# Kernel optimization log

Hardware: AMD Instinct MI355X
Metric: run time of the kernel (lower is better)

Reference implementation:

```python
import jax, jax.numpy as jnp
import numpy as np

RADIUS = 400.0
FIELD = 8000.0  # um extent of slide coordinate field


def setup_inputs() -> dict:
    key = jax.random.key(0)
    ks = jax.random.split(key, 8)
    B, N, D, H, K = 4, 4096, 1536, 512, 8
    images = jax.random.normal(ks[0], (B, N, D), dtype=jnp.float32)
    positions = jax.random.uniform(ks[1], (B, N, 2), dtype=jnp.float32) * FIELD
    W_feat = jax.random.normal(ks[2], (D, H), dtype=jnp.float32) * (1.0 / np.sqrt(D))
    b_feat = jnp.zeros((H,), dtype=jnp.float32)
    W_pos = jax.random.normal(ks[3], (2, H), dtype=jnp.float32) * 0.5
    W_gnn = jax.random.normal(ks[4], (H, H), dtype=jnp.float32) * (1.0 / np.sqrt(H))
    W_self = jax.random.normal(ks[5], (H, H), dtype=jnp.float32) * (1.0 / np.sqrt(H))
    anchors = jax.random.normal(ks[6], (K, D), dtype=jnp.float32)
    return {"images": images, "positions": positions, "W_feat": W_feat,
            "b_feat": b_feat, "W_pos": W_pos, "W_gnn": W_gnn,
            "W_self": W_self, "anchors": anchors}


def _radius_adjacency(pos):
    # pos: (N, 2). Dense O(N^2) radius graph (mirrors torch.cdist + mask).
    sq = jnp.sum(pos * pos, axis=-1)                       # (N,)
    d2 = sq[:, None] + sq[None, :] - 2.0 * (pos @ pos.T)   # (N, N)
    mask = d2 < (RADIUS * RADIUS)
    N = pos.shape[0]
    mask = mask & ~jnp.eye(N, dtype=bool)                  # no self-loops
    return mask.astype(pos.dtype)


def reference(images, positions, W_feat, b_feat, W_pos, W_gnn, W_self, anchors):
    # --- Stream A: explicit concept quantifier (cosine sim to anchors) ---
    x_norm = images / jnp.clip(jnp.linalg.norm(images, axis=-1, keepdims=True), 1e-12)
    a_norm = anchors / jnp.clip(jnp.linalg.norm(anchors, axis=-1, keepdims=True), 1e-12)
    scores = jnp.einsum('bnd,kd->bnk', x_norm, a_norm)     # (B, N, K)
    concept_profile = scores.mean(axis=1)                  # (B, K)

    # --- Stream B: feature extraction with positional encoding ---
    feat = images @ W_feat + b_feat + positions @ W_pos    # (B, N, H)

    # --- radius graph + one mean-aggregation GNN layer, per slide ---
    def per_graph(f, p):
        A = _radius_adjacency(p)                           # (N, N)
        deg = jnp.clip(A.sum(axis=-1, keepdims=True), 1.0) # (N, 1)
        h = jax.nn.relu(f)
        agg = (A @ h) / deg                                # mean over neighbors
        return jax.nn.relu(agg @ W_gnn + f @ W_self)       # (N, H)

    refined = jax.vmap(per_graph)(feat, positions)         # (B, N, H)
    latent_spatial = refined.mean(axis=1)                  # (B, H)  per-graph mean pool

    return jnp.concatenate([latent_spatial, concept_profile], axis=1)  # (B, H+K)
```

## Files before the change

kernel.cpp:

```cpp
#include <hip/hip_runtime.h>

#define B_ 4
#define N_ 4096
#define D_ 1536
#define H_ 512
#define K_ 8
#define M_ (B_*N_)
#define R2_ 160000.0f
#define CAP 192

typedef __attribute__((ext_vector_type(8))) short bf16x8;
typedef __attribute__((ext_vector_type(4))) float f32x4;
typedef __attribute__((ext_vector_type(2))) float f32x2;

__device__ __forceinline__ unsigned short f2bf(float f) {
  union { float f; unsigned u; } v; v.f = f;
  unsigned r = (v.u + 0x7FFFu + ((v.u >> 16) & 1u)) >> 16;
  return (unsigned short)r;
}

typedef const __attribute__((address_space(1))) unsigned int gas_u32;
typedef __attribute__((address_space(3))) unsigned int las_u32;
__device__ __forceinline__ void gl_lds16(const unsigned short* g, unsigned short* l) {
  __builtin_amdgcn_global_load_lds((gas_u32*)g, (las_u32*)l, 16, 0, 0);
}

#define CAST_BLKS 4096

__global__ __launch_bounds__(256) void k_prepcast(
    const float* __restrict__ images, const float* __restrict__ anchors,
    const float* __restrict__ Wf, const float* __restrict__ Wg, const float* __restrict__ Ws,
    unsigned short* __restrict__ imgs_bf, float* __restrict__ inv_norm,
    unsigned short* __restrict__ WfT, unsigned short* __restrict__ WgsT,
    unsigned short* __restrict__ ancT, float* __restrict__ invanorm) {
  int tid = threadIdx.x;
  if (blockIdx.x >= CAST_BLKS) {
    int bi = blockIdx.x - CAST_BLKS;
    if (bi < 320) {
      __shared__ float t[64][65];
      int bx = bi & 7, by = bi >> 3;
      const float* W; unsigned short* WT; int kt, outStride, outOff;
      if (by < 24)      { W = Wf; WT = WfT;  kt = by;      outStride = D_;   outOff = 0; }
      else if (by < 32) { W = Wg; WT = WgsT; kt = by - 24; outStride = 1024; outOff = 0; }
      else              { W = Ws; WT = WgsT; kt = by - 32; outStride = 1024; outOff = 512; }
      int tx = tid & 63, ty = tid >> 6;
      #pragma unroll
      for (int r = 0; r < 64; r += 4)
        t[ty + r][tx] = W[(size_t)(kt*64 + ty + r)*H_ + bx*64 + tx];
      __syncthreads();
      #pragma unroll
      for (int r = 0; r < 64; r += 4) {
        int n = bx*64 + ty + r;
        WT[(size_t)n*outStride + outOff + kt*64 + tx] = f2bf(t[tx][ty + r]);
      }
      return;
    }
    __shared__ float red[4];
    int k = bi - 320;
    float s = 0.f;
    for (int i = tid; i < D_; i += 256) {
      float v = anchors[k*D_ + i];
      s += v*v;
      ancT[(size_t)k*D_ + i] = f2bf(v);
      ancT[(size_t)(k+8)*D_ + i] = 0;
    }
    #pragma unroll
    for (int off = 32; off; off >>= 1) s += __shfl_down(s, off);
    if ((tid & 63) == 0) red[tid >> 6] = s;
    __syncthreads();
    if (tid == 0) invanorm[k] = 1.0f / fmaxf(sqrtf(red[0]+red[1]+red[2]+red[3]), 1e-12f);
    return;
  }
  int lane = tid & 63, w = tid >> 6;
  int row = blockIdx.x*4 + w;
  const float4* xr = (const float4*)(images + (size_t)row*D_);
  ushort4* ob = (ushort4*)(imgs_bf + (size_t)row*D_);
  float nrm = 0.f;
  #pragma unroll
  for (int it = 0; it < 6; it++) {
    float4 x = xr[lane + 64*it];
    nrm += x.x*x.x + x.y*x.y + x.z*x.z + x.w*x.w;
    ushort4 s;
    s.x = f2bf(x.x); s.y = f2bf(x.y); s.z = f2bf(x.z); s.w = f2bf(x.w);
    ob[lane + 64*it] = s;
  }
  #pragma unroll
  for (int off = 32; off; off >>= 1) nrm += __shfl_down(nrm, off);
  if (lane == 0) inv_norm[row] = 1.0f / fmaxf(sqrtf(nrm), 1e-12f);
}

#define BM 128
#define BN 128
#define BK 32

__global__ __launch_bounds__(256) void k_gemm(
    const unsigned short* __restrict__ A, const unsigned short* __restrict__ BT,
    int Kdim, int mode, const float* __restrict__ bias, const float* __restrict__ Wpos,
    const float* __restrict__ positions, unsigned short* __restrict__ AB,
    unsigned char* __restrict__ P, const unsigned short* __restrict__ ancT,
    const float* __restrict__ invnorm, const float* __restrict__ invanorm,
    float* __restrict__ out) {
  __shared__ __align__(16) unsigned short As[2][BM*BK];
  __shared__ __align__(16) unsigned short Bs[2][BN*BK];
  __shared__ float colsum[BN];
  int tid = threadIdx.x;
  int lane = tid & 63, wv = tid >> 6;
  int l15 = lane & 15, quad = lane >> 4;
  int bx = blockIdx.x;

  int wm = wv >> 1, wn = wv & 1;
  int j = bx >> 3;
  int bm = (bx & 7) + 8*(j >> 2), bn = j & 3;
  int m0 = bm*BM, n0 = bn*BN;

  const bool doC = (mode == 0) && (bn == 0);

  f32x4 acc[4][4] = {};
  f32x4 cacc[2] = {};
  const unsigned short* anc = ancT + l15*D_ + quad*8;

  int c = wv*2;
  int rowc = (lane >> 2), seg = lane & 3;
  const unsigned short* gA0 = A  + (size_t)(m0 + c*16 + rowc)*Kdim + seg*8;
  const unsigned short* gA1 = gA0 + (size_t)16*Kdim;
  const unsigned short* gB0 = BT + (size_t)(n0 + c*16 + rowc)*Kdim + seg*8;
  const unsigned short* gB1 = gB0 + (size_t)16*Kdim;

  int nk = Kdim / BK;
  gl_lds16(gA0, As[0] + c*512); gl_lds16(gA1, As[0] + c*512 + 512);
  gl_lds16(gB0, Bs[0] + c*512); gl_lds16(gB1, Bs[0] + c*512 + 512);
  gA0 += BK; gA1 += BK; gB0 += BK; gB1 += BK;
  __syncthreads();

  int cur = 0;
  for (int kt = 0; kt < nk; kt++) {
    if (kt + 1 < nk) {
      unsigned short* nA = As[cur ^ 1] + c*512;
      unsigned short* nB = Bs[cur ^ 1] + c*512;
      gl_lds16(gA0, nA); gl_lds16(gA1, nA + 512);
      gl_lds16(gB0, nB); gl_lds16(gB1, nB + 512);
      gA0 += BK; gA1 += BK; gB0 += BK; gB1 += BK;
    }

    const unsigned short* Ab = As[cur];
    const unsigned short* Bb = Bs[cur];
    bf16x8 aF[4], bF[4];
    #pragma unroll
    for (int f = 0; f < 4; f++)
      aF[f] = *(const bf16x8*)&Ab[(wm*64 + f*16 + l15)*BK + quad*8];
    #pragma unroll
    for (int f = 0; f < 4; f++)
      bF[f] = *(const bf16x8*)&Bb[(wn*64 + f*16 + l15)*BK + quad*8];
    #pragma unroll
    for (int mi = 0; mi < 4; mi++)
      #pragma unroll
      for (int ni = 0; ni < 4; ni++)
        acc[mi][ni] = __builtin_amdgcn_mfma_f32_16x16x32_bf16(aF[mi], bF[ni], acc[mi][ni], 0, 0, 0);

    if (doC) {
      bf16x8 ancF = *(const bf16x8*)anc;
      anc += BK;
      if (wn == 0) {
        cacc[0] = __builtin_amdgcn_mfma_f32_16x16x32_bf16(aF[0], ancF, cacc[0], 0, 0, 0);
        cacc[1] = __builtin_amdgcn_mfma_f32_16x16x32_bf16(aF[1], ancF, cacc[1], 0, 0, 0);
      } else {
        cacc[0] = __builtin_amdgcn_mfma_f32_16x16x32_bf16(aF[2], ancF, cacc[0], 0, 0, 0);
        cacc[1] = __builtin_amdgcn_mfma_f32_16x16x32_bf16(aF[3], ancF, cacc[1], 0, 0, 0);
      }
    }

    __syncthreads();
    cur ^= 1;
  }

  if (doC) {
    float invA = (l15 < K_) ? invanorm[l15] : 0.f;
    float part = 0.f;
    #pragma unroll
    for (int f = 0; f < 2; f++) {
      const float4 q = *(const float4*)&invnorm[m0 + wm*64 + wn*32 + f*16 + quad*4];
      part += cacc[f][0]*q.x + cacc[f][1]*q.y + cacc[f][2]*q.z + cacc[f][3]*q.w;
    }
    part *= invA;
    part += __shfl_down(part, 32);
    part += __shfl_down(part, 16);
    if (lane < K_) atomicAdd(out + (m0 >> 12)*(H_+K_) + H_ + lane, part * (1.0f/N_));
  }

  if (mode == 0) {
    float bz[4], w0v[4], w1v[4];
    #pragma unroll
    for (int ni = 0; ni < 4; ni++) {
      int gh = n0 + wn*64 + ni*16 + l15;
      bz[ni] = bias[gh]; w0v[ni] = Wpos[gh]; w1v[ni] = Wpos[H_ + gh];
    }
    float* sb = ((float*)As[0]) + wv*256;
    int col4 = n0 + wn*64 + l15*4;
    #pragma unroll
    for (int mi = 0; mi < 4; mi++) {
      #pragma unroll
      for (int r = 0; r < 4; r++) {
        int gm = m0 + wm*64 + mi*16 + quad*4 + r;
        float2 p = ((const float2*)positions)[gm];
        #pragma unroll
        for (int ni = 0; ni < 4; ni++) {
          float v = acc[mi][ni][r] + bz[ni] + p.x*w0v[ni] + p.y*w1v[ni];
          sb[quad*64 + ni*16 + l15] = v;
        }
        f32x4 q = *(f32x4*)&sb[quad*64 + l15*4];
        uint2 o;
        o.x = ((unsigned)f2bf(q[1]) << 16) | f2bf(q[0]);
        o.y = ((unsigned)f2bf(q[3]) << 16) | f2bf(q[2]);
        *(uint2*)&AB[(size_t)gm*1024 + 512 + col4] = o;
        float e0 = fminf(fmaxf(q[0], 0.f)*0.015625f, 448.f);
        float e1 = fminf(fmaxf(q[1], 0.f)*0.015625f, 448.f);
        float e2 = fminf(fmaxf(q[2], 0.f)*0.015625f, 448.f);
        float e3 = fminf(fmaxf(q[3], 0.f)*0.015625f, 448.f);
        int u = __builtin_amdgcn_cvt_pk_fp8_f32(e0, e1, 0, false);
        u     = __builtin_amdgcn_cvt_pk_fp8_f32(e2, e3, u, true);
        *(unsigned*)(P + (size_t)gm*512 + col4) = (unsigned)u;
      }
    }
  } else {
    if (tid < BN) colsum[tid] = 0.f;
    __syncthreads();
    #pragma unroll
    for (int ni = 0; ni < 4; ni++) {
      float s = 0.f;
      #pragma unroll
      for (int mi = 0; mi < 4; mi++) {
        #pragma unroll
        for (int r = 0; r < 4; r++) s += fmaxf(acc[mi][ni][r], 0.f);
      }
      s += __shfl_down(s, 32);
      s += __shfl_down(s, 16);
      if (quad == 0) atomicAdd(&colsum[wn*64 + ni*16 + l15], s);
    }
    __syncthreads();
    if (tid < BN) {
      int b = m0 >> 12;
      atomicAdd(out + b*(H_+K_) + n0 + tid, colsum[tid] * (1.0f/N_));
    }
  }
}

__device__ __forceinline__ void accf8(uint2 v, float* a) {
  f32x2 p;
  p = __builtin_amdgcn_cvt_pk_f32_fp8(v.x, false); a[0] += p[0]; a[1] += p[1];
  p = __builtin_amdgcn_cvt_pk_f32_fp8(v.x, true);  a[2] += p[0]; a[3] += p[1];
  p = __builtin_amdgcn_cvt_pk_f32_fp8(v.y, false); a[4] += p[0]; a[5] += p[1];
  p = __builtin_amdgcn_cvt_pk_f32_fp8(v.y, true);  a[6] += p[0]; a[7] += p[1];
}

__global__ __launch_bounds__(256) void k_aggregate(const float* __restrict__ positions,
                                                   const unsigned char* __restrict__ P,
                                                   unsigned short* __restrict__ AB) {
  __shared__ unsigned short nl[8*CAP];
  __shared__ int cnt[8];
  __shared__ float sdx[8], sdy[8];
  int blk = blockIdx.x;
  int xcd = blk & 7;
  int b = xcd >> 1;
  int sub = ((blk >> 3) << 1) | (xcd & 1);
  int dest0 = sub * 8;
  int tid = threadIdx.x, lane = tid & 63, w = tid >> 6;
  const float2* p2 = (const float2*)(positions + (size_t)b*N_*2);
  if (tid < 8) {
    cnt[tid] = 0;
    float2 pd = p2[dest0 + tid];
    sdx[tid] = pd.x; sdy[tid] = pd.y;
  }
  __syncthreads();
  for (int it = 0; it < 16; it++) {
    int j = tid + 256*it;
    float2 pj = p2[j];
    #pragma unroll
    for (int d = 0; d < 8; d++) {
      float dx = pj.x - sdx[d], dy = pj.y - sdy[d];
      if (dx*dx + dy*dy < R2_ && j != dest0 + d) {
        int p = atomicAdd(&cnt[d], 1);
        if (p < CAP) nl[d*CAP + p] = (unsigned short)j;
      }
    }
  }
  __syncthreads();
  const unsigned char* featb = P + ((size_t)(b << 12))*512 + lane*8;
  #pragma unroll
  for (int dd = 0; dd < 2; dd++) {
    int d = w*2 + dd;
    int deg = cnt[d]; if (deg > CAP) deg = CAP;
    float inv = 64.0f / (float)(deg > 1 ? deg : 1);
    const unsigned short* nlp = &nl[d*CAP];
    float a[8] = {};
    int n = 0;
    for (; n + 4 <= deg; n += 4) {
      ushort4 idx = *(const ushort4*)&nlp[n];
      uint2 v0 = *(const uint2*)(featb + (size_t)idx.x*512);
      uint2 v1 = *(const uint2*)(featb + (size_t)idx.y*512);
      uint2 v2 = *(const uint2*)(featb + (size_t)idx.z*512);
      uint2 v3 = *(const uint2*)(featb + (size_t)idx.w*512);
      accf8(v0, a); accf8(v1, a); accf8(v2, a); accf8(v3, a);
    }
    for (; n < deg; n++) {
      int j = nlp[n];
      uint2 v = *(const uint2*)(featb + (size_t)j*512);
      accf8(v, a);
    }
    uint4 o;
    o.x = ((unsigned)f2bf(a[1]*inv) << 16) | f2bf(a[0]*inv);
    o.y = ((unsigned)f2bf(a[3]*inv) << 16) | f2bf(a[2]*inv);
    o.z = ((unsigned)f2bf(a[5]*inv) << 16) | f2bf(a[4]*inv);
    o.w = ((unsigned)f2bf(a[7]*inv) << 16) | f2bf(a[6]*inv);
    *(uint4*)(AB + (size_t)((b << 12) + dest0 + d)*1024 + lane*8) = o;
  }
}

extern "C" void kernel_launch(void* const* d_in, const int* in_sizes, int n_in,
                              void* d_out, int out_size, void* d_ws, size_t ws_size,
                              hipStream_t stream) {
  const float* images    = (const float*)d_in[0];
  const float* positions = (const float*)d_in[1];
  const float* W_feat    = (const float*)d_in[2];
  const float* b_feat    = (const float*)d_in[3];
  const float* W_pos     = (const float*)d_in[4];
  const float* W_gnn     = (const float*)d_in[5];
  const float* W_self    = (const float*)d_in[6];
  const float* anchors   = (const float*)d_in[7];
  float* out = (float*)d_out;

  char* ws = (char*)d_ws;
  unsigned short* imgs_bf = (unsigned short*)ws;
  unsigned short* AB      = (unsigned short*)(ws + 50331648);
  unsigned short* WfT     = (unsigned short*)(ws + 83886080);
  unsigned short* WgsT    = (unsigned short*)(ws + 85458944);
  unsigned char*  P       = (unsigned char*)(ws + 86507520);
  float*          invanorm= (float*)(ws + 94896128);
  unsigned short* ancT    = (unsigned short*)(ws + 94896160);
  float*          inv_norm= (float*)(ws + 94945312);

  hipMemsetAsync(d_out, 0, sizeof(float)*B_*(H_+K_), stream);
  k_prepcast<<<CAST_BLKS + 320 + 8, 256, 0, stream>>>(images, anchors, W_feat, W_gnn, W_self,
                                                      imgs_bf, inv_norm, WfT, WgsT, ancT, invanorm);
  k_gemm<<<512, 256, 0, stream>>>(imgs_bf, WfT, D_, 0, b_feat, W_pos, positions, AB, P,
                                  ancT, inv_norm, invanorm, out);
  k_aggregate<<<2048, 256, 0, stream>>>(positions, P, AB);
  k_gemm<<<512, 256, 0, stream>>>(AB, WgsT, 1024, 1, nullptr, nullptr, nullptr, AB, nullptr,
                                  ancT, inv_norm, invanorm, out);
}
```

Baseline: 274.7 us.

## Triple-buffer GEMM LDS pipeline with explicit vmcnt waits and anchor prefetch

```diff
diff --git a/kernel.cpp b/kernel.cpp
--- a/kernel.cpp
+++ b/kernel.cpp
@@ -100,8 +100,8 @@
     unsigned char* __restrict__ P, const unsigned short* __restrict__ ancT,
     const float* __restrict__ invnorm, const float* __restrict__ invanorm,
     float* __restrict__ out) {
-  __shared__ __align__(16) unsigned short As[2][BM*BK];
-  __shared__ __align__(16) unsigned short Bs[2][BN*BK];
+  __shared__ __align__(16) unsigned short As[3][BM*BK];
+  __shared__ __align__(16) unsigned short Bs[3][BN*BK];
   __shared__ float colsum[BN];
   int tid = threadIdx.x;
   int lane = tid & 63, wv = tid >> 6;
@@ -126,24 +126,39 @@
   const unsigned short* gB0 = BT + (size_t)(n0 + c*16 + rowc)*Kdim + seg*8;
   const unsigned short* gB1 = gB0 + (size_t)16*Kdim;
 
+#define STAGE(b) do { \
+    unsigned short* nA = As[b] + c*512; \
+    unsigned short* nB = Bs[b] + c*512; \
+    gl_lds16(gA0, nA); gl_lds16(gA1, nA + 512); \
+    gl_lds16(gB0, nB); gl_lds16(gB1, nB + 512); \
+    gA0 += BK; gA1 += BK; gB0 += BK; gB1 += BK; } while (0)
+
   int nk = Kdim / BK;
-  gl_lds16(gA0, As[0] + c*512); gl_lds16(gA1, As[0] + c*512 + 512);
-  gl_lds16(gB0, Bs[0] + c*512); gl_lds16(gB1, Bs[0] + c*512 + 512);
-  gA0 += BK; gA1 += BK; gB0 += BK; gB1 += BK;
-  __syncthreads();
-
-  int cur = 0;
+  union { uint4 u; bf16x8 h; } ancCur, ancNext;
+  if (doC)
+    asm volatile("global_load_dwordx4 %0, %1, off" : "=v"(ancNext.u) : "v"(anc) : "memory");
+  STAGE(0);
+  STAGE(1);
+  const unsigned short* ancp = anc + BK;
+
+  int cb = 0, nb = 2;
   for (int kt = 0; kt < nk; kt++) {
-    if (kt + 1 < nk) {
-      unsigned short* nA = As[cur ^ 1] + c*512;
-      unsigned short* nB = Bs[cur ^ 1] + c*512;
-      gl_lds16(gA0, nA); gl_lds16(gA1, nA + 512);
-      gl_lds16(gB0, nB); gl_lds16(gB1, nB + 512);
-      gA0 += BK; gA1 += BK; gB0 += BK; gB1 += BK;
-    }
-
-    const unsigned short* Ab = As[cur];
-    const unsigned short* Bb = Bs[cur];
+    if (kt + 1 < nk) asm volatile("s_waitcnt vmcnt(4)" ::: "memory");
+    else             asm volatile("s_waitcnt vmcnt(0)" ::: "memory");
+    __builtin_amdgcn_s_barrier();
+    asm volatile("" ::: "memory");
+
+    ancCur = ancNext;
+    if (doC && kt + 1 < nk) {
+      asm volatile("global_load_dwordx4 %0, %1, off" : "=v"(ancNext.u) : "v"(ancp) : "memory");
+      ancp += BK;
+    }
+    if (kt + 2 < nk) { STAGE(nb); nb = (nb + 1 == 3) ? 0 : nb + 1; }
+
+    const unsigned short* Ab = As[cb];
+    const unsigned short* Bb = Bs[cb];
+    cb = (cb + 1 == 3) ? 0 : cb + 1;
+
     bf16x8 aF[4], bF[4];
     #pragma unroll
     for (int f = 0; f < 4; f++)
@@ -158,8 +173,7 @@
         acc[mi][ni] = __builtin_amdgcn_mfma_f32_16x16x32_bf16(aF[mi], bF[ni], acc[mi][ni], 0, 0, 0);
 
     if (doC) {
-      bf16x8 ancF = *(const bf16x8*)anc;
-      anc += BK;
+      bf16x8 ancF = ancCur.h;
       if (wn == 0) {
         cacc[0] = __builtin_amdgcn_mfma_f32_16x16x32_bf16(aF[0], ancF, cacc[0], 0, 0, 0);
         cacc[1] = __builtin_amdgcn_mfma_f32_16x16x32_bf16(aF[1], ancF, cacc[1], 0, 0, 0);
@@ -168,10 +182,8 @@
         cacc[1] = __builtin_amdgcn_mfma_f32_16x16x32_bf16(aF[3], ancF, cacc[1], 0, 0, 0);
       }
     }
-
-    __syncthreads();
-    cur ^= 1;
-  }
+  }
+#undef STAGE
 
   if (doC) {
     float invA = (l15 < K_) ? invanorm[l15] : 0.f;
```

New measurement: 275.0 us. About the same (+0.1%).
